# Optimization experiments

Measured on AMD Instinct MI355X. Metric: run time of the kernel, lower is better.

The kernel has to match this reference:

```python
import jax, jax.numpy as jnp
import numpy as np

C_A = 768; C_S = 384; C_Z = 128; H = 16; D = C_A // H
B = 1; N = 4096; NQ = 32; NK = 128; NB = N // NQ
EPS = 1e-5


def _ln(x):
    # layernorm without learned affine (affine applied by caller where present)
    m = jnp.mean(x, axis=-1, keepdims=True)
    v = jnp.mean((x - m) ** 2, axis=-1, keepdims=True)
    return (x - m) * jax.lax.rsqrt(v + EPS)


def setup_inputs() -> dict:
    key = jax.random.key(0)
    ks = jax.random.split(key, 16)
    w = lambda k, shp: jax.random.normal(k, shp, dtype=jnp.float32) * 0.02
    return dict(
        a=jax.random.normal(ks[0], (B, N, C_A), jnp.float32),
        s=jax.random.normal(ks[1], (B, N, C_S), jnp.float32),
        z=jax.random.normal(ks[2], (B, NB, NQ, NK, C_Z), jnp.float32),
        adaln_gamma_s=jnp.ones((C_S,), jnp.float32),
        adaln_ws=w(ks[3], (C_S, C_A)),
        adaln_bs=jnp.zeros((C_A,), jnp.float32),
        adaln_wskip=w(ks[4], (C_S, C_A)),
        lnz_gamma=jnp.ones((C_Z,), jnp.float32),
        wz=w(ks[5], (C_Z, H)),
        wq=w(ks[6], (C_A, C_A)), bq=jnp.zeros((C_A,), jnp.float32),
        wk=w(ks[7], (C_A, C_A)),
        wv=w(ks[8], (C_A, C_A)),
        wg=w(ks[9], (C_A, C_A)), bg=jnp.ones((C_A,), jnp.float32),
        wo=w(ks[10], (C_A, C_A)), bo=jnp.zeros((C_A,), jnp.float32),
        w_last=w(ks[11], (C_S, C_A)),
        b_last=jnp.full((C_A,), -2.0, jnp.float32),  # biasinit = -2.0
        n_queries=NQ, n_keys=NK,
    )


def _forward(a, s, z, adaln_gamma_s, adaln_ws, adaln_bs, adaln_wskip,
             lnz_gamma, wz, wq, bq, wk, wv, wg, bg, wo, bo,
             w_last, b_last, n_queries, n_keys):
    Bq, Nq, _ = a.shape
    nb = Nq // n_queries
    # AdaptiveLayerNorm (AF3 Alg 26): a <- sigmoid(Lin(s_ln)) * LN(a) + LinNoBias(s_ln)
    s_ln = _ln(s) * adaln_gamma_s
    a_ln = jax.nn.sigmoid(s_ln @ adaln_ws + adaln_bs) * _ln(a) + s_ln @ adaln_wskip
    # pair bias: LN(z) (no offset) -> per-head bias, permuted to [B,H,nb,nq,nk]
    bias = (_ln(z) * lnz_gamma) @ wz                    # [B, nb, nq, nk, H]
    bias = jnp.transpose(bias, (0, 4, 1, 2, 3))          # [B, H, nb, nq, nk]
    # projections (q has bias; k/v no bias)
    q = (a_ln @ wq + bq).reshape(Bq, nb, n_queries, H, D)
    k = (a_ln @ wk).reshape(Bq, Nq, H, D)
    v = (a_ln @ wv).reshape(Bq, Nq, H, D)
    # local window: query block w covers [w*nq, (w+1)*nq); keys are nk centered on it
    start = jnp.arange(nb) * n_queries + n_queries // 2 - n_keys // 2
    kidx = start[:, None] + jnp.arange(n_keys)[None, :]  # [nb, nk]
    valid = (kidx >= 0) & (kidx < Nq)
    kidx = jnp.clip(kidx, 0, Nq - 1)
    k_loc = k[:, kidx]                                    # [B, nb, nk, H, D]
    v_loc = v[:, kidx]
    scale = 1.0 / float(np.sqrt(D))
    scores = jnp.einsum('bwqhd,bwkhd->bhwqk', q, k_loc) * scale + bias
    scores = jnp.where(valid[None, None, :, None, :], scores, -1e9)
    p = jax.nn.softmax(scores, axis=-1)
    o = jnp.einsum('bhwqk,bwkhd->bwqhd', p, v_loc).reshape(Bq, Nq, C_A)
    # gating, output projection, final sigmoid gate from raw s
    o = (jax.nn.sigmoid(a_ln @ wg + bg) * o) @ wo + bo
    return jax.nn.sigmoid(s @ w_last + b_last) * o


def reference(a, s, z, adaln_gamma_s, adaln_ws, adaln_bs, adaln_wskip,
              lnz_gamma, wz, wq, bq, wk, wv, wg, bg, wo, bo,
              w_last, b_last, n_queries, n_keys):
    return _forward(a, s, z, adaln_gamma_s, adaln_ws, adaln_bs, adaln_wskip,
                    lnz_gamma, wz, wq, bq, wk, wv, wg, bg, wo, bo,
                    w_last, b_last, n_queries, n_keys)
```

## Files before the change

kernel.cpp:

```cpp
#include <hip/hip_runtime.h>
#include <hip/hip_bf16.h>
#include <math.h>

#define N_TOK 4096
#define CA 768
#define CS 384
#define CZ 128
#define NHEAD 16
#define DH 48
#define NQW 32
#define NKW 128
#define NBLK 128

typedef __attribute__((ext_vector_type(8))) short short8;
typedef __attribute__((ext_vector_type(4))) float float4v;
typedef __attribute__((ext_vector_type(4))) unsigned short ushort4v;

__device__ __forceinline__ float sigmoidf_(float x){ return 1.0f/(1.0f+__expf(-x)); }

__device__ __forceinline__ unsigned short f2bf(float x){
  unsigned u = __float_as_uint(x);
  unsigned r = (u + 0x7FFFu + ((u>>16)&1u)) >> 16;
  return (unsigned short)r;
}
__device__ __forceinline__ float bf2f(unsigned short b){
  return __uint_as_float(((unsigned)b)<<16);
}
__device__ __forceinline__ short8 cvt8(const float* xv){
  union { short8 v; unsigned short u[8]; } H;
  #pragma unroll
  for (int j=0;j<8;j++) H.u[j] = f2bf(xv[j]);
  return H.v;
}
__device__ __forceinline__ short8 cvt8pk(const float* x){
  union { short8 v; unsigned u32[4]; } H;
  #pragma unroll
  for (int i=0;i<4;i++)
    asm("v_cvt_pk_bf16_f32 %0, %1, %2" : "=v"(H.u32[i]) : "v"(x[2*i]), "v"(x[2*i+1]));
  return H.v;
}

__device__ __forceinline__ void gload_lds16(const void* gsrc, void* ldst){
  __builtin_amdgcn_global_load_lds(
    (const __attribute__((address_space(1))) void*)gsrc,
    (__attribute__((address_space(3))) void*)ldst, 16, 0, 0);
}

__device__ __forceinline__ int xcd_swz(int wg, int nwg){
  int cpx = nwg >> 3;
  return (wg & 7)*cpx + (wg >> 3);
}

__global__ __launch_bounds__(256) void prep_zbias_kernel(
  const float* __restrict__ z, const float* __restrict__ lnz_gamma,
  const float* __restrict__ wz, unsigned short* __restrict__ bias3,
  const float* __restrict__ s, const float* __restrict__ adaln_gamma,
  unsigned short* __restrict__ s_ln_h, unsigned short* __restrict__ s_h,
  const float* __restrict__ a, float* __restrict__ a_n,
  const float* __restrict__ ws, const float* __restrict__ wskip,
  const float* __restrict__ wq, const float* __restrict__ wk,
  const float* __restrict__ wv, const float* __restrict__ wg,
  const float* __restrict__ wo, const float* __restrict__ wlast,
  unsigned short* __restrict__ Wt1, unsigned short* __restrict__ Wt2,
  unsigned short* __restrict__ Wt3, unsigned short* __restrict__ Wt4,
  const float* __restrict__ bq, const float* __restrict__ bg,
  float* __restrict__ biasq)
{
  union PZ {
    float tile[64][65];
    float zbuf[4][2][2048];
  };
  __shared__ PZ sm;
  int bid = blockIdx.x;
  int tid = threadIdx.x;

  if (bid < 1024){
    int wave = tid>>6, lane = tid&63;
    int lr = lane&15, quad = lane>>4;

    short8 bwh[4];
    float w1 = 0.f;
    #pragma unroll
    for (int ks=0;ks<4;ks++){
      float wv_[8];
      #pragma unroll
      for (int j=0;j<8;j++){
        int k = ks*32 + quad*8 + j;
        wv_[j] = wz[k*NHEAD + lr]*lnz_gamma[k];
        w1 += wv_[j];
      }
      bwh[ks] = cvt8pk(wv_);
    }
    w1 += __shfl_xor(w1, 16);
    w1 += __shfl_xor(w1, 32);

    size_t group = (size_t)bid*4 + wave;
    const float* zg = z + group*(size_t)(NKW*CZ);
    unsigned short* outg = bias3 + group*2048;

    int rsub = lane>>5;
    int csw  = lane&31;
    auto stage = [&](int buf, int b){
      #pragma unroll
      for (int i=0;i<8;i++){
        int r  = 2*i + rsub;
        int gc = csw ^ (r & 7);
        gload_lds16(zg + (size_t)(b*16 + r)*CZ + gc*4, &sm.zbuf[wave][buf][i*256]);
      }
    };

    stage(0, 0);
    int buf = 0;
    #pragma unroll 1
    for (int b=0; b<8; ++b){
      if (b < 7){
        stage(buf^1, b+1);
        asm volatile("s_waitcnt vmcnt(8)" ::: "memory");
      } else {
        asm volatile("s_waitcnt vmcnt(0)" ::: "memory");
      }
      __builtin_amdgcn_sched_barrier(0);

      const float* rowp = &sm.zbuf[wave][buf][lr*128];
      int sswz = lr & 7;
      float4 p[8];
      #pragma unroll
      for (int ks=0;ks<4;ks++){
        int c0 = ks*8 + quad*2;
        p[ks*2]   = *(const float4*)(rowp + (size_t)((c0  )^sswz)*4);
        p[ks*2+1] = *(const float4*)(rowp + (size_t)((c0+1)^sswz)*4);
      }
      float sum=0.f, sq=0.f;
      #pragma unroll
      for (int t=0;t<8;t++){
        sum += p[t].x + p[t].y + p[t].z + p[t].w;
        sq  += p[t].x*p[t].x + p[t].y*p[t].y + p[t].z*p[t].z + p[t].w*p[t].w;
      }
      sum += __shfl_xor(sum,16); sum += __shfl_xor(sum,32);
      sq  += __shfl_xor(sq,16);  sq  += __shfl_xor(sq,32);
      float mean = sum*(1.f/CZ);
      float var  = sq*(1.f/CZ) - mean*mean;
      float rs = rsqrtf(var + 1e-5f);

      float4v c = (float4v){0.f,0.f,0.f,0.f};
      #pragma unroll
      for (int ks=0;ks<4;ks++){
        float xv[8];
        xv[0]=p[ks*2].x;   xv[1]=p[ks*2].y;   xv[2]=p[ks*2].z;   xv[3]=p[ks*2].w;
        xv[4]=p[ks*2+1].x; xv[5]=p[ks*2+1].y; xv[6]=p[ks*2+1].z; xv[7]=p[ks*2+1].w;
        c = __builtin_amdgcn_mfma_f32_16x16x32_bf16(cvt8pk(xv), bwh[ks], c, 0,0,0);
      }

      ushort4v o4;
      #pragma unroll
      for (int r=0;r<4;r++){
        int rrow = quad*4 + r;
        float m_r  = __shfl(mean, rrow);
        float rs_r = __shfl(rs, rrow);
        o4[r] = f2bf(rs_r*(c[r] - m_r*w1));
      }
      *(ushort4v*)(outg + lr*128 + b*16 + quad*4) = o4;
      buf ^= 1;
    }
    return;
  }
  bid -= 1024;

  if (bid < 1024){
    int wave = tid>>6, lane = tid&63;
    int row = bid*4 + wave;
    const float* x = s + (size_t)row*CS;
    float v[6]; float sum=0.f, sq=0.f;
    #pragma unroll
    for (int i=0;i<6;i++){ v[i]=x[lane+64*i]; sum+=v[i]; sq+=v[i]*v[i]; }
    #pragma unroll
    for (int off=32; off; off>>=1){ sum+=__shfl_xor(sum,off); sq+=__shfl_xor(sq,off); }
    float m = sum*(1.f/CS);
    float var = sq*(1.f/CS)-m*m;
    float rs = rsqrtf(var+1e-5f);
    #pragma unroll
    for (int i=0;i<6;i++){
      int c = lane+64*i;
      s_ln_h[(size_t)row*CS+c] = f2bf((v[i]-m)*rs*adaln_gamma[c]);
      s_h[(size_t)row*CS+c]    = f2bf(v[i]);
    }
    return;
  }
  bid -= 1024;

  if (bid < 1024){
    int wave = tid>>6, lane = tid&63;
    int row = bid*4 + wave;
    const float* x = a + (size_t)row*CA;
    float v[12]; float sum=0.f, sq=0.f;
    #pragma unroll
    for (int i=0;i<12;i++){ v[i]=x[lane+64*i]; sum+=v[i]; sq+=v[i]*v[i]; }
    #pragma unroll
    for (int off=32; off; off>>=1){ sum+=__shfl_xor(sum,off); sq+=__shfl_xor(sq,off); }
    float m = sum*(1.f/CA);
    float var = sq*(1.f/CA)-m*m;
    float rs = rsqrtf(var+1e-5f);
    float* o = a_n + (size_t)row*CA;
    #pragma unroll
    for (int i=0;i<12;i++) o[lane+64*i] = (v[i]-m)*rs;
    return;
  }
  bid -= 1024;

  if (bid < 936){
    const float* src; unsigned short* dst; int K; int local;
    if      (bid < 72)  { src=ws;    dst=Wt1;                   K=CS; local=bid; }
    else if (bid < 144) { src=wskip; dst=Wt1 + (size_t)768*CS;  K=CS; local=bid-72; }
    else if (bid < 288) { src=wq;    dst=Wt2;                   K=CA; local=bid-144; }
    else if (bid < 432) { src=wk;    dst=Wt2 + (size_t)768*CA;  K=CA; local=bid-288; }
    else if (bid < 576) { src=wv;    dst=Wt2 + (size_t)1536*CA; K=CA; local=bid-432; }
    else if (bid < 720) { src=wg;    dst=Wt2 + (size_t)2304*CA; K=CA; local=bid-576; }
    else if (bid < 864) { src=wo;    dst=Wt3;                   K=CA; local=bid-720; }
    else                { src=wlast; dst=Wt4;                   K=CS; local=bid-864; }
    int ktiles = K/64;
    int kb = (local % ktiles)*64, nb = (local / ktiles)*64;
    int c = tid & 63, r0 = tid >> 6;
    #pragma unroll
    for (int i=0;i<16;i++){
      int r = r0 + 4*i;
      sm.tile[r][c] = src[(size_t)(kb+r)*CA + nb + c];
    }
    __syncthreads();
    #pragma unroll
    for (int i=0;i<16;i++){
      int r = r0 + 4*i;
      dst[(size_t)(nb+r)*K + kb + c] = f2bf(sm.tile[c][r]);
    }
    return;
  }
  bid -= 936;

  int i = bid*256 + tid;
  float v = 0.f;
  if (i < 768) v = bq[i];
  else if (i >= 2304) v = bg[i-2304];
  biasq[i] = v;
}

__global__ __launch_bounds__(256) void adaln_gemm(
  const unsigned short* __restrict__ A, const unsigned short* __restrict__ Bt,
  const float* __restrict__ bs, const float* __restrict__ a_n,
  unsigned short* __restrict__ outh)
{
  __shared__ unsigned short Ash[128*32];
  __shared__ unsigned short B1sh[128*32];
  __shared__ unsigned short B2sh[128*32];

  int tid = threadIdx.x;
  int w = tid >> 6, lane = tid & 63;
  int lr = lane & 15, quad = lane >> 4;
  int wg = xcd_swz(blockIdx.y*gridDim.x + blockIdx.x, gridDim.x*gridDim.y);
  int bx = wg % gridDim.x, by = wg / gridDim.x;
  int m0 = by*128, n0 = bx*128;
  int mbase = (w&1)*64, nbase = (w>>1)*64;

  float4v acc1[4][4], acc2[4][4];
  #pragma unroll
  for (int i=0;i<4;i++)
    #pragma unroll
    for (int j=0;j<4;j++){
      acc1[i][j] = (float4v){0.f,0.f,0.f,0.f};
      acc2[i][j] = (float4v){0.f,0.f,0.f,0.f};
    }

  int grow = w*32 + (lane>>2);
  int gcol8 = (lane&3)*8;

  for (int k0=0; k0<CS; k0+=32){
    __syncthreads();
    #pragma unroll
    for (int i=0;i<2;i++){
      int rA = grow + i*16;
      gload_lds16(A  + (size_t)(m0 + rA)*CS + k0 + gcol8, &Ash[(w*32 + i*16)*32]);
      gload_lds16(Bt + (size_t)(n0 + rA)*CS + k0 + gcol8, &B1sh[(w*32 + i*16)*32]);
      gload_lds16(Bt + (size_t)(768 + n0 + rA)*CS + k0 + gcol8, &B2sh[(w*32 + i*16)*32]);
    }
    __syncthreads();

    short8 af[4], b1f[4], b2f[4];
    #pragma unroll
    for (int mi=0;mi<4;mi++)
      af[mi] = *(const short8*)&Ash[(mbase + mi*16 + lr)*32 + quad*8];
    #pragma unroll
    for (int ni=0;ni<4;ni++){
      b1f[ni] = *(const short8*)&B1sh[(nbase + ni*16 + lr)*32 + quad*8];
      b2f[ni] = *(const short8*)&B2sh[(nbase + ni*16 + lr)*32 + quad*8];
    }
    #pragma unroll
    for (int mi=0;mi<4;mi++)
      #pragma unroll
      for (int ni=0;ni<4;ni++){
        acc1[mi][ni] = __builtin_amdgcn_mfma_f32_16x16x32_bf16(af[mi], b1f[ni], acc1[mi][ni], 0,0,0);
        acc2[mi][ni] = __builtin_amdgcn_mfma_f32_16x16x32_bf16(af[mi], b2f[ni], acc2[mi][ni], 0,0,0);
      }
  }

  #pragma unroll
  for (int ni=0;ni<4;ni++){
    int col = n0 + nbase + ni*16 + lr;
    float bsv = bs[col];
    #pragma unroll
    for (int mi=0;mi<4;mi++){
      #pragma unroll
      for (int reg=0;reg<4;reg++){
        int row = m0 + mbase + mi*16 + quad*4 + reg;
        float v = sigmoidf_(acc1[mi][ni][reg] + bsv)*a_n[(size_t)row*CA + col] + acc2[mi][ni][reg];
        outh[(size_t)row*CA + col] = f2bf(v);
      }
    }
  }
}

template<int MODE>
__global__ __launch_bounds__(256) void gemm_bf16(
  const unsigned short* __restrict__ A1, const unsigned short* __restrict__ B1,
  const float* __restrict__ bias1, int K1,
  const unsigned short* __restrict__ A2, const unsigned short* __restrict__ B2,
  const float* __restrict__ bias2, int K2,
  void* __restrict__ outp, int M, int N)
{
  __shared__ unsigned short Ash[128*32];
  __shared__ unsigned short Bsh[128*32];

  int tid = threadIdx.x;
  int w = tid >> 6, lane = tid & 63;
  int lr = lane & 15, quad = lane >> 4;
  int wg = xcd_swz(blockIdx.y*gridDim.x + blockIdx.x, gridDim.x*gridDim.y);
  int bx = wg % gridDim.x, by = wg / gridDim.x;
  int m0 = by*128, n0 = bx*128;
  int mbase = (w&1)*64, nbase = (w>>1)*64;

  float4v acc1[4][4];
  float4v acc2[4][4];
  #pragma unroll
  for (int i=0;i<4;i++)
    #pragma unroll
    for (int j=0;j<4;j++){
      acc1[i][j] = (float4v){0.f,0.f,0.f,0.f};
      if constexpr (MODE == 3) acc2[i][j] = (float4v){0.f,0.f,0.f,0.f};
    }

  int grow = w*32 + (lane>>2);
  int gcol8 = (lane&3)*8;

  for (int k0=0; k0<K1; k0+=32){
    __syncthreads();
    #pragma unroll
    for (int i=0;i<2;i++){
      int rA = grow + i*16;
      gload_lds16(A1 + (size_t)(m0 + rA)*K1 + k0 + gcol8, &Ash[(w*32 + i*16)*32]);
      gload_lds16(B1 + (size_t)(n0 + rA)*K1 + k0 + gcol8, &Bsh[(w*32 + i*16)*32]);
    }
    __syncthreads();

    short8 af[4], bf[4];
    #pragma unroll
    for (int mi=0;mi<4;mi++)
      af[mi] = *(const short8*)&Ash[(mbase + mi*16 + lr)*32 + quad*8];
    #pragma unroll
    for (int ni=0;ni<4;ni++)
      bf[ni] = *(const short8*)&Bsh[(nbase + ni*16 + lr)*32 + quad*8];
    #pragma unroll
    for (int mi=0;mi<4;mi++)
      #pragma unroll
      for (int ni=0;ni<4;ni++)
        acc1[mi][ni] = __builtin_amdgcn_mfma_f32_16x16x32_bf16(af[mi], bf[ni], acc1[mi][ni], 0,0,0);
  }

  if constexpr (MODE == 3){
    for (int k0=0; k0<K2; k0+=32){
      __syncthreads();
      #pragma unroll
      for (int i=0;i<2;i++){
        int rA = grow + i*16;
        gload_lds16(A2 + (size_t)(m0 + rA)*K2 + k0 + gcol8, &Ash[(w*32 + i*16)*32]);
        gload_lds16(B2 + (size_t)(n0 + rA)*K2 + k0 + gcol8, &Bsh[(w*32 + i*16)*32]);
      }
      __syncthreads();

      short8 af[4], bf[4];
      #pragma unroll
      for (int mi=0;mi<4;mi++)
        af[mi] = *(const short8*)&Ash[(mbase + mi*16 + lr)*32 + quad*8];
      #pragma unroll
      for (int ni=0;ni<4;ni++)
        bf[ni] = *(const short8*)&Bsh[(nbase + ni*16 + lr)*32 + quad*8];
      #pragma unroll
      for (int mi=0;mi<4;mi++)
        #pragma unroll
        for (int ni=0;ni<4;ni++)
          acc2[mi][ni] = __builtin_amdgcn_mfma_f32_16x16x32_bf16(af[mi], bf[ni], acc2[mi][ni], 0,0,0);
    }
  }

  #pragma unroll
  for (int ni=0;ni<4;ni++){
    int col = n0 + nbase + ni*16 + lr;
    float bv1 = bias1 ? bias1[col] : 0.f;
    float bv2 = (MODE==3 && bias2) ? bias2[col] : 0.f;
    #pragma unroll
    for (int mi=0;mi<4;mi++){
      #pragma unroll
      for (int reg=0;reg<4;reg++){
        int row = m0 + mbase + mi*16 + quad*4 + reg;
        float x1 = acc1[mi][ni][reg] + bv1;
        if constexpr (MODE == 1)
          ((unsigned short*)outp)[(size_t)row*N + col] = f2bf(x1);
        else
          ((float*)outp)[(size_t)row*N + col] = sigmoidf_(acc2[mi][ni][reg] + bv2)*x1;
      }
    }
  }
}

__global__ __launch_bounds__(256) void attn_kernel(
  const unsigned short* __restrict__ qh,
  const unsigned short* __restrict__ bias3h,
  unsigned short* __restrict__ og)
{
  __shared__ unsigned short Vs[128*192];
  __shared__ unsigned short Pb[4][32*40];
  int tid = threadIdx.x, wave = tid>>6, lane = tid&63;
  int lr = lane&15, quad = lane>>4;
  int w = blockIdx.x, h = blockIdx.y*4 + wave;
  int start = w*NQW - 48;
  const float scale = 0.14433756729740643f;

  {
    int hbase = blockIdx.y*4*DH;
    #pragma unroll
    for (int it=0; it<12; ++it){
      int c = it*256 + tid;
      int key = c/24, cc = c - key*24;
      int kr = min(max(start+key,0),N_TOK-1);
      short8 v = *(const short8*)&qh[(size_t)kr*3072 + 1536 + hbase + cc*8];
      int cs = cc ^ (((key>>3)&3)*2);
      *(short8*)&Vs[key*192 + cs*8] = v;
    }
  }

  short8 zero8 = {0,0,0,0,0,0,0,0};

  short8 aq[2][2];
  #pragma unroll
  for (int mt=0;mt<2;mt++){
    int row = w*NQW + mt*16 + lr;
    const unsigned short* qp = qh + (size_t)row*3072 + h*DH;
    aq[mt][0] = *(const short8*)(qp + quad*8);
    aq[mt][1] = (quad<2) ? *(const short8*)(qp + 32 + quad*8) : zero8;
  }

  float4v c[2][8];
  #pragma unroll
  for (int mt=0;mt<2;mt++)
    #pragma unroll
    for (int nt=0;nt<8;nt++) c[mt][nt] = (float4v){0.f,0.f,0.f,0.f};

  #pragma unroll 2
  for (int nt=0;nt<8;nt++){
    int krc = min(max(start + nt*16 + lr,0),N_TOK-1);
    const unsigned short* kp = qh + (size_t)krc*3072 + 768 + h*DH;
    short8 bk0 = *(const short8*)(kp + quad*8);
    short8 bk1 = (quad<2) ? *(const short8*)(kp + 32 + quad*8) : zero8;
    #pragma unroll
    for (int mt=0;mt<2;mt++){
      c[mt][nt] = __builtin_amdgcn_mfma_f32_16x16x32_bf16(aq[mt][0], bk0, c[mt][nt], 0,0,0);
      c[mt][nt] = __builtin_amdgcn_mfma_f32_16x16x32_bf16(aq[mt][1], bk1, c[mt][nt], 0,0,0);
    }
  }

  float rmax[2][4], rsum[2][4];
  #pragma unroll
  for (int mt=0;mt<2;mt++)
    #pragma unroll
    for (int r=0;r<4;r++){ rmax[mt][r] = -3.0e38f; rsum[mt][r] = 0.f; }

  #pragma unroll
  for (int nt=0;nt<8;nt++){
    int key = start + nt*16 + lr;
    bool valid = (key>=0) && (key<N_TOK);
    #pragma unroll
    for (int mt=0;mt<2;mt++){
      #pragma unroll
      for (int r=0;r<4;r++){
        int q = mt*16 + quad*4 + r;
        float bv = bf2f(bias3h[(((size_t)(w*NQW+q))*NHEAD + h)*128 + nt*16 + lr]);
        float v = valid ? (c[mt][nt][r]*scale + bv) : -1e9f;
        c[mt][nt][r] = v;
        rmax[mt][r] = fmaxf(rmax[mt][r], v);
      }
    }
  }
  #pragma unroll
  for (int mt=0;mt<2;mt++)
    #pragma unroll
    for (int r=0;r<4;r++){
      float m = rmax[mt][r];
      m = fmaxf(m, __shfl_xor(m,1)); m = fmaxf(m, __shfl_xor(m,2));
      m = fmaxf(m, __shfl_xor(m,4)); m = fmaxf(m, __shfl_xor(m,8));
      rmax[mt][r] = m;
    }
  #pragma unroll
  for (int nt=0;nt<8;nt++)
    #pragma unroll
    for (int mt=0;mt<2;mt++)
      #pragma unroll
      for (int r=0;r<4;r++){
        float e = __expf(c[mt][nt][r] - rmax[mt][r]);
        c[mt][nt][r] = e;
        rsum[mt][r] += e;
      }
  #pragma unroll
  for (int mt=0;mt<2;mt++)
    #pragma unroll
    for (int r=0;r<4;r++){
      float sv = rsum[mt][r];
      sv += __shfl_xor(sv,1); sv += __shfl_xor(sv,2);
      sv += __shfl_xor(sv,4); sv += __shfl_xor(sv,8);
      rsum[mt][r] = 1.f/sv;
    }

  __syncthreads();

  unsigned short* ph = &Pb[wave][0];
  float4v o[2][3];
  #pragma unroll
  for (int mt=0;mt<2;mt++)
    #pragma unroll
    for (int no=0;no<3;no++) o[mt][no] = (float4v){0.f,0.f,0.f,0.f};

  #pragma unroll 1
  for (int c2=0;c2<2;c2++){
    #pragma unroll 1
    for (int ks=0;ks<2;ks++){
      int ntb = c2*4 + ks*2;
      #pragma unroll
      for (int t=0;t<2;t++){
        int nt = ntb + t;
        #pragma unroll
        for (int mt=0;mt<2;mt++){
          #pragma unroll
          for (int r=0;r<4;r++){
            int q = mt*16 + quad*4 + r;
            ph[q*40 + t*16 + lr] = f2bf(c[mt][nt][r]*rsum[mt][r]);
          }
        }
      }
      short8 pa[2];
      #pragma unroll
      for (int mt=0;mt<2;mt++)
        pa[mt] = *(const short8*)&ph[(mt*16+lr)*40 + quad*8];
      #pragma unroll
      for (int no=0;no<3;no++){
        union { short8 v; unsigned short u[8]; } V;
        int col = wave*DH + no*16 + lr;
        int chunk = col >> 3;
        int cs = (chunk ^ (quad*2))*8 + (col & 7);
        #pragma unroll
        for (int j=0;j<8;j++){
          int key = c2*64 + ks*32 + quad*8 + j;
          V.u[j] = Vs[key*192 + cs];
        }
        #pragma unroll
        for (int mt=0;mt<2;mt++)
          o[mt][no] = __builtin_amdgcn_mfma_f32_16x16x32_bf16(pa[mt], V.v, o[mt][no], 0,0,0);
      }
    }
  }

  #pragma unroll
  for (int mt=0;mt<2;mt++){
    #pragma unroll
    for (int no=0;no<3;no++){
      int d = no*16 + lr;
      #pragma unroll
      for (int r=0;r<4;r++){
        int q = mt*16 + quad*4 + r;
        size_t grow = (size_t)(w*NQW + q);
        float g = bf2f(qh[grow*3072 + 2304 + h*DH + d]);
        og[grow*CA + h*DH + d] = f2bf(o[mt][no][r] * sigmoidf_(g));
      }
    }
  }
}

extern "C" void kernel_launch(void* const* d_in, const int* in_sizes, int n_in,
                              void* d_out, int out_size, void* d_ws, size_t ws_size,
                              hipStream_t stream)
{
  const float* a            = (const float*)d_in[0];
  const float* s            = (const float*)d_in[1];
  const float* z            = (const float*)d_in[2];
  const float* adaln_gamma  = (const float*)d_in[3];
  const float* adaln_ws     = (const float*)d_in[4];
  const float* adaln_bs     = (const float*)d_in[5];
  const float* adaln_wskip  = (const float*)d_in[6];
  const float* lnz_gamma    = (const float*)d_in[7];
  const float* wz           = (const float*)d_in[8];
  const float* wq           = (const float*)d_in[9];
  const float* bq           = (const float*)d_in[10];
  const float* wk           = (const float*)d_in[11];
  const float* wv           = (const float*)d_in[12];
  const float* wg           = (const float*)d_in[13];
  const float* bg           = (const float*)d_in[14];
  const float* wo           = (const float*)d_in[15];
  const float* bo           = (const float*)d_in[16];
  const float* w_last       = (const float*)d_in[17];
  const float* b_last       = (const float*)d_in[18];
  float* out = (float*)d_out;

  char* base = (char*)d_ws;
  size_t off = 0;
  auto alloc = [&](size_t bytes)->char*{ char* p = base + off; off += (bytes + 255) & ~(size_t)255; return p; };

  unsigned short* s_ln_h = (unsigned short*)alloc((size_t)N_TOK*CS*2);
  unsigned short* s_h    = (unsigned short*)alloc((size_t)N_TOK*CS*2);
  float*          a_n    = (float*)alloc((size_t)N_TOK*CA*4);
  unsigned short* a_ln_h = (unsigned short*)alloc((size_t)N_TOK*CA*2);
  unsigned short* og_h   = (unsigned short*)alloc((size_t)N_TOK*CA*2);
  unsigned short* Wt1    = (unsigned short*)alloc((size_t)1536*CS*2);
  unsigned short* Wt2    = (unsigned short*)alloc((size_t)3072*CA*2);
  unsigned short* Wt3    = (unsigned short*)alloc((size_t)CA*CA*2);
  unsigned short* Wt4    = (unsigned short*)alloc((size_t)CA*CS*2);
  unsigned short* bias3h = (unsigned short*)alloc((size_t)N_TOK*NHEAD*NKW*2);
  unsigned short* qkvg_h = (unsigned short*)alloc((size_t)N_TOK*3072*2);
  float*          biasq  = (float*)alloc((size_t)3072*4);

  prep_zbias_kernel<<<dim3(1024+1024+1024+936+12), 256, 0, stream>>>(
      z, lnz_gamma, wz, bias3h,
      s, adaln_gamma, s_ln_h, s_h, a, a_n,
      adaln_ws, adaln_wskip, wq, wk, wv, wg, wo, w_last,
      Wt1, Wt2, Wt3, Wt4, bq, bg, biasq);

  adaln_gemm<<<dim3(CA/128, N_TOK/128), 256, 0, stream>>>(s_ln_h, Wt1, adaln_bs, a_n, a_ln_h);

  gemm_bf16<1><<<dim3(3072/128, N_TOK/128), 256, 0, stream>>>(
      a_ln_h, Wt2, biasq, CA, nullptr, nullptr, nullptr, 0, qkvg_h, N_TOK, 3072);

  attn_kernel<<<dim3(NBLK, 4), 256, 0, stream>>>(qkvg_h, bias3h, og_h);

  gemm_bf16<3><<<dim3(CA/128, N_TOK/128), 256, 0, stream>>>(
      og_h, Wt3, bo, CA, s_h, Wt4, b_last, CS, out, N_TOK, CA);
}
```

Baseline: 232.8 us.

## Halve GEMM M-tiles for more blocks and split z-bias groups across blocks

The adaln and final GEMMs switch from 128x128 to 64x128 tiles, which doubles the grid from 192 to 384 blocks so more of the GPU's compute units are busy. The final GEMM now merges both K loops into a single loop with a branch. The z-bias prep section now runs with twice as many blocks, and only 2 of the 4 waves in each block do work, which is meant to raise occupancy through the smaller LDS footprint. The QKVG GEMM is specialized with fixed constants. The risks are less data reuse per tile and half-idle blocks in the prep kernel.

Result: faster. 221.0 us (-5.1%).

```diff
diff --git a/kernel.cpp b/kernel.cpp
--- a/kernel.cpp
+++ b/kernel.cpp
@@ -68,14 +68,15 @@
 {
   union PZ {
     float tile[64][65];
-    float zbuf[4][2][2048];
+    float zbuf[2][2][2048];
   };
   __shared__ PZ sm;
   int bid = blockIdx.x;
   int tid = threadIdx.x;
 
-  if (bid < 1024){
+  if (bid < 2048){
     int wave = tid>>6, lane = tid&63;
+    if (wave >= 2) return;
     int lr = lane&15, quad = lane>>4;
 
     short8 bwh[4];
@@ -94,7 +95,7 @@
     w1 += __shfl_xor(w1, 16);
     w1 += __shfl_xor(w1, 32);
 
-    size_t group = (size_t)bid*4 + wave;
+    size_t group = (size_t)bid*2 + wave;
     const float* zg = z + group*(size_t)(NKW*CZ);
     unsigned short* outg = bias3 + group*2048;
 
@@ -164,7 +165,7 @@
     }
     return;
   }
-  bid -= 1024;
+  bid -= 2048;
 
   if (bid < 1024){
     int wave = tid>>6, lane = tid&63;
@@ -247,9 +248,166 @@
   const float* __restrict__ bs, const float* __restrict__ a_n,
   unsigned short* __restrict__ outh)
 {
-  __shared__ unsigned short Ash[128*32];
+  __shared__ unsigned short Ash[64*32];
   __shared__ unsigned short B1sh[128*32];
   __shared__ unsigned short B2sh[128*32];
+
+  int tid = threadIdx.x;
+  int w = tid >> 6, lane = tid & 63;
+  int lr = lane & 15, quad = lane >> 4;
+  int wg = xcd_swz(blockIdx.y*gridDim.x + blockIdx.x, gridDim.x*gridDim.y);
+  int bx = wg % gridDim.x, by = wg / gridDim.x;
+  int m0 = by*64, n0 = bx*128;
+  int mbase = (w&1)*32, nbase = (w>>1)*64;
+
+  float4v acc1[2][4], acc2[2][4];
+  #pragma unroll
+  for (int i=0;i<2;i++)
+    #pragma unroll
+    for (int j=0;j<4;j++){
+      acc1[i][j] = (float4v){0.f,0.f,0.f,0.f};
+      acc2[i][j] = (float4v){0.f,0.f,0.f,0.f};
+    }
+
+  int growB = w*32 + (lane>>2);
+  int growA = w*16 + (lane>>2);
+  int gcol8 = (lane&3)*8;
+
+  for (int k0=0; k0<CS; k0+=32){
+    __syncthreads();
+    gload_lds16(A + (size_t)(m0 + growA)*CS + k0 + gcol8, &Ash[(w*16)*32]);
+    #pragma unroll
+    for (int i=0;i<2;i++){
+      int rB = growB + i*16;
+      gload_lds16(Bt + (size_t)(n0 + rB)*CS + k0 + gcol8, &B1sh[(w*32 + i*16)*32]);
+      gload_lds16(Bt + (size_t)(768 + n0 + rB)*CS + k0 + gcol8, &B2sh[(w*32 + i*16)*32]);
+    }
+    __syncthreads();
+
+    short8 af[2], b1f[4], b2f[4];
+    #pragma unroll
+    for (int mi=0;mi<2;mi++)
+      af[mi] = *(const short8*)&Ash[(mbase + mi*16 + lr)*32 + quad*8];
+    #pragma unroll
+    for (int ni=0;ni<4;ni++){
+      b1f[ni] = *(const short8*)&B1sh[(nbase + ni*16 + lr)*32 + quad*8];
+      b2f[ni] = *(const short8*)&B2sh[(nbase + ni*16 + lr)*32 + quad*8];
+    }
+    #pragma unroll
+    for (int mi=0;mi<2;mi++)
+      #pragma unroll
+      for (int ni=0;ni<4;ni++){
+        acc1[mi][ni] = __builtin_amdgcn_mfma_f32_16x16x32_bf16(af[mi], b1f[ni], acc1[mi][ni], 0,0,0);
+        acc2[mi][ni] = __builtin_amdgcn_mfma_f32_16x16x32_bf16(af[mi], b2f[ni], acc2[mi][ni], 0,0,0);
+      }
+  }
+
+  #pragma unroll
+  for (int ni=0;ni<4;ni++){
+    int col = n0 + nbase + ni*16 + lr;
+    float bsv = bs[col];
+    #pragma unroll
+    for (int mi=0;mi<2;mi++){
+      #pragma unroll
+      for (int reg=0;reg<4;reg++){
+        int row = m0 + mbase + mi*16 + quad*4 + reg;
+        float v = sigmoidf_(acc1[mi][ni][reg] + bsv)*a_n[(size_t)row*CA + col] + acc2[mi][ni][reg];
+        outh[(size_t)row*CA + col] = f2bf(v);
+      }
+    }
+  }
+}
+
+__global__ __launch_bounds__(256) void final_gemm(
+  const unsigned short* __restrict__ A1, const unsigned short* __restrict__ B1,
+  const float* __restrict__ bias1,
+  const unsigned short* __restrict__ A2, const unsigned short* __restrict__ B2,
+  const float* __restrict__ bias2,
+  float* __restrict__ outp)
+{
+  __shared__ unsigned short Ash[64*32];
+  __shared__ unsigned short Bsh[128*32];
+
+  int tid = threadIdx.x;
+  int w = tid >> 6, lane = tid & 63;
+  int lr = lane & 15, quad = lane >> 4;
+  int wg = xcd_swz(blockIdx.y*gridDim.x + blockIdx.x, gridDim.x*gridDim.y);
+  int bx = wg % gridDim.x, by = wg / gridDim.x;
+  int m0 = by*64, n0 = bx*128;
+  int mbase = (w&1)*32, nbase = (w>>1)*64;
+
+  float4v acc1[2][4], acc2[2][4];
+  #pragma unroll
+  for (int i=0;i<2;i++)
+    #pragma unroll
+    for (int j=0;j<4;j++){
+      acc1[i][j] = (float4v){0.f,0.f,0.f,0.f};
+      acc2[i][j] = (float4v){0.f,0.f,0.f,0.f};
+    }
+
+  int growB = w*32 + (lane>>2);
+  int growA = w*16 + (lane>>2);
+  int gcol8 = (lane&3)*8;
+
+  const int NT1 = CA/32, NT2 = CS/32, NT = NT1+NT2;
+  #pragma unroll 1
+  for (int t=0; t<NT; ++t){
+    const unsigned short* Ap; const unsigned short* Bp; int K, k0;
+    if (t < NT1){ Ap=A1; Bp=B1; K=CA; k0=t*32; }
+    else        { Ap=A2; Bp=B2; K=CS; k0=(t-NT1)*32; }
+    __syncthreads();
+    gload_lds16(Ap + (size_t)(m0 + growA)*K + k0 + gcol8, &Ash[(w*16)*32]);
+    #pragma unroll
+    for (int i=0;i<2;i++){
+      int rB = growB + i*16;
+      gload_lds16(Bp + (size_t)(n0 + rB)*K + k0 + gcol8, &Bsh[(w*32 + i*16)*32]);
+    }
+    __syncthreads();
+
+    short8 af[2], bf[4];
+    #pragma unroll
+    for (int mi=0;mi<2;mi++)
+      af[mi] = *(const short8*)&Ash[(mbase + mi*16 + lr)*32 + quad*8];
+    #pragma unroll
+    for (int ni=0;ni<4;ni++)
+      bf[ni] = *(const short8*)&Bsh[(nbase + ni*16 + lr)*32 + quad*8];
+    if (t < NT1){
+      #pragma unroll
+      for (int mi=0;mi<2;mi++)
+        #pragma unroll
+        for (int ni=0;ni<4;ni++)
+          acc1[mi][ni] = __builtin_amdgcn_mfma_f32_16x16x32_bf16(af[mi], bf[ni], acc1[mi][ni], 0,0,0);
+    } else {
+      #pragma unroll
+      for (int mi=0;mi<2;mi++)
+        #pragma unroll
+        for (int ni=0;ni<4;ni++)
+          acc2[mi][ni] = __builtin_amdgcn_mfma_f32_16x16x32_bf16(af[mi], bf[ni], acc2[mi][ni], 0,0,0);
+    }
+  }
+
+  #pragma unroll
+  for (int ni=0;ni<4;ni++){
+    int col = n0 + nbase + ni*16 + lr;
+    float bv1 = bias1[col];
+    float bv2 = bias2[col];
+    #pragma unroll
+    for (int mi=0;mi<2;mi++){
+      #pragma unroll
+      for (int reg=0;reg<4;reg++){
+        int row = m0 + mbase + mi*16 + quad*4 + reg;
+        outp[(size_t)row*CA + col] = sigmoidf_(acc2[mi][ni][reg] + bv2)*(acc1[mi][ni][reg] + bv1);
+      }
+    }
+  }
+}
+
+__global__ __launch_bounds__(256) void qkvg_gemm(
+  const unsigned short* __restrict__ A1, const unsigned short* __restrict__ B1,
+  const float* __restrict__ bias1, unsigned short* __restrict__ outp)
+{
+  __shared__ unsigned short Ash[128*32];
+  __shared__ unsigned short Bsh[128*32];
 
   int tid = threadIdx.x;
   int w = tid >> 6, lane = tid & 63;
@@ -259,160 +417,50 @@
   int m0 = by*128, n0 = bx*128;
   int mbase = (w&1)*64, nbase = (w>>1)*64;
 
-  float4v acc1[4][4], acc2[4][4];
+  float4v acc1[4][4];
   #pragma unroll
   for (int i=0;i<4;i++)
     #pragma unroll
-    for (int j=0;j<4;j++){
+    for (int j=0;j<4;j++)
       acc1[i][j] = (float4v){0.f,0.f,0.f,0.f};
-      acc2[i][j] = (float4v){0.f,0.f,0.f,0.f};
-    }
 
   int grow = w*32 + (lane>>2);
   int gcol8 = (lane&3)*8;
 
-  for (int k0=0; k0<CS; k0+=32){
+  for (int k0=0; k0<CA; k0+=32){
     __syncthreads();
     #pragma unroll
     for (int i=0;i<2;i++){
       int rA = grow + i*16;
-      gload_lds16(A  + (size_t)(m0 + rA)*CS + k0 + gcol8, &Ash[(w*32 + i*16)*32]);
-      gload_lds16(Bt + (size_t)(n0 + rA)*CS + k0 + gcol8, &B1sh[(w*32 + i*16)*32]);
-      gload_lds16(Bt + (size_t)(768 + n0 + rA)*CS + k0 + gcol8, &B2sh[(w*32 + i*16)*32]);
+      gload_lds16(A1 + (size_t)(m0 + rA)*CA + k0 + gcol8, &Ash[(w*32 + i*16)*32]);
+      gload_lds16(B1 + (size_t)(n0 + rA)*CA + k0 + gcol8, &Bsh[(w*32 + i*16)*32]);
     }
     __syncthreads();
 
-    short8 af[4], b1f[4], b2f[4];
+    short8 af[4], bf[4];
     #pragma unroll
     for (int mi=0;mi<4;mi++)
       af[mi] = *(const short8*)&Ash[(mbase + mi*16 + lr)*32 + quad*8];
     #pragma unroll
-    for (int ni=0;ni<4;ni++){
-      b1f[ni] = *(const short8*)&B1sh[(nbase + ni*16 + lr)*32 + quad*8];
-      b2f[ni] = *(const short8*)&B2sh[(nbase + ni*16 + lr)*32 + quad*8];
-    }
+    for (int ni=0;ni<4;ni++)
+      bf[ni] = *(const short8*)&Bsh[(nbase + ni*16 + lr)*32 + quad*8];
     #pragma unroll
     for (int mi=0;mi<4;mi++)
       #pragma unroll
-      for (int ni=0;ni<4;ni++){
-        acc1[mi][ni] = __builtin_amdgcn_mfma_f32_16x16x32_bf16(af[mi], b1f[ni], acc1[mi][ni], 0,0,0);
-        acc2[mi][ni] = __builtin_amdgcn_mfma_f32_16x16x32_bf16(af[mi], b2f[ni], acc2[mi][ni], 0,0,0);
-      }
+      for (int ni=0;ni<4;ni++)
+        acc1[mi][ni] = __builtin_amdgcn_mfma_f32_16x16x32_bf16(af[mi], bf[ni], acc1[mi][ni], 0,0,0);
   }
 
   #pragma unroll
   for (int ni=0;ni<4;ni++){
     int col = n0 + nbase + ni*16 + lr;
-    float bsv = bs[col];
+    float bv = bias1[col];
     #pragma unroll
     for (int mi=0;mi<4;mi++){
       #pragma unroll
       for (int reg=0;reg<4;reg++){
         int row = m0 + mbase + mi*16 + quad*4 + reg;
-        float v = sigmoidf_(acc1[mi][ni][reg] + bsv)*a_n[(size_t)row*CA + col] + acc2[mi][ni][reg];
-        outh[(size_t)row*CA + col] = f2bf(v);
-      }
-    }
-  }
-}
-
-template<int MODE>
-__global__ __launch_bounds__(256) void gemm_bf16(
-  const unsigned short* __restrict__ A1, const unsigned short* __restrict__ B1,
-  const float* __restrict__ bias1, int K1,
-  const unsigned short* __restrict__ A2, const unsigned short* __restrict__ B2,
-  const float* __restrict__ bias2, int K2,
-  void* __restrict__ outp, int M, int N)
-{
-  __shared__ unsigned short Ash[128*32];
-  __shared__ unsigned short Bsh[128*32];
-
-  int tid = threadIdx.x;
-  int w = tid >> 6, lane = tid & 63;
-  int lr = lane & 15, quad = lane >> 4;
-  int wg = xcd_swz(blockIdx.y*gridDim.x + blockIdx.x, gridDim.x*gridDim.y);
-  int bx = wg % gridDim.x, by = wg / gridDim.x;
-  int m0 = by*128, n0 = bx*128;
-  int mbase = (w&1)*64, nbase = (w>>1)*64;
-
-  float4v acc1[4][4];
-  float4v acc2[4][4];
-  #pragma unroll
-  for (int i=0;i<4;i++)
-    #pragma unroll
-    for (int j=0;j<4;j++){
-      acc1[i][j] = (float4v){0.f,0.f,0.f,0.f};
-      if constexpr (MODE == 3) acc2[i][j] = (float4v){0.f,0.f,0.f,0.f};
-    }
-
-  int grow = w*32 + (lane>>2);
-  int gcol8 = (lane&3)*8;
-
-  for (int k0=0; k0<K1; k0+=32){
-    __syncthreads();
-    #pragma unroll
-    for (int i=0;i<2;i++){
-      int rA = grow + i*16;
-      gload_lds16(A1 + (size_t)(m0 + rA)*K1 + k0 + gcol8, &Ash[(w*32 + i*16)*32]);
-      gload_lds16(B1 + (size_t)(n0 + rA)*K1 + k0 + gcol8, &Bsh[(w*32 + i*16)*32]);
-    }
-    __syncthreads();
-
-    short8 af[4], bf[4];
-    #pragma unroll
-    for (int mi=0;mi<4;mi++)
-      af[mi] = *(const short8*)&Ash[(mbase + mi*16 + lr)*32 + quad*8];
-    #pragma unroll
-    for (int ni=0;ni<4;ni++)
-      bf[ni] = *(const short8*)&Bsh[(nbase + ni*16 + lr)*32 + quad*8];
-    #pragma unroll
-    for (int mi=0;mi<4;mi++)
-      #pragma unroll
-      for (int ni=0;ni<4;ni++)
-        acc1[mi][ni] = __builtin_amdgcn_mfma_f32_16x16x32_bf16(af[mi], bf[ni], acc1[mi][ni], 0,0,0);
-  }
-
-  if constexpr (MODE == 3){
-    for (int k0=0; k0<K2; k0+=32){
-      __syncthreads();
-      #pragma unroll
-      for (int i=0;i<2;i++){
-        int rA = grow + i*16;
-        gload_lds16(A2 + (size_t)(m0 + rA)*K2 + k0 + gcol8, &Ash[(w*32 + i*16)*32]);
-        gload_lds16(B2 + (size_t)(n0 + rA)*K2 + k0 + gcol8, &Bsh[(w*32 + i*16)*32]);
-      }
-      __syncthreads();
-
-      short8 af[4], bf[4];
-      #pragma unroll
-      for (int mi=0;mi<4;mi++)
-        af[mi] = *(const short8*)&Ash[(mbase + mi*16 + lr)*32 + quad*8];
-      #pragma unroll
-      for (int ni=0;ni<4;ni++)
-        bf[ni] = *(const short8*)&Bsh[(nbase + ni*16 + lr)*32 + quad*8];
-      #pragma unroll
-      for (int mi=0;mi<4;mi++)
-        #pragma unroll
-        for (int ni=0;ni<4;ni++)
-          acc2[mi][ni] = __builtin_amdgcn_mfma_f32_16x16x32_bf16(af[mi], bf[ni], acc2[mi][ni], 0,0,0);
-    }
-  }
-
-  #pragma unroll
-  for (int ni=0;ni<4;ni++){
-    int col = n0 + nbase + ni*16 + lr;
-    float bv1 = bias1 ? bias1[col] : 0.f;
-    float bv2 = (MODE==3 && bias2) ? bias2[col] : 0.f;
-    #pragma unroll
-    for (int mi=0;mi<4;mi++){
-      #pragma unroll
-      for (int reg=0;reg<4;reg++){
-        int row = m0 + mbase + mi*16 + quad*4 + reg;
-        float x1 = acc1[mi][ni][reg] + bv1;
-        if constexpr (MODE == 1)
-          ((unsigned short*)outp)[(size_t)row*N + col] = f2bf(x1);
-        else
-          ((float*)outp)[(size_t)row*N + col] = sigmoidf_(acc2[mi][ni][reg] + bv2)*x1;
+        outp[(size_t)row*3072 + col] = f2bf(acc1[mi][ni][reg] + bv);
       }
     }
   }
@@ -631,19 +679,18 @@
   unsigned short* qkvg_h = (unsigned short*)alloc((size_t)N_TOK*3072*2);
   float*          biasq  = (float*)alloc((size_t)3072*4);
 
-  prep_zbias_kernel<<<dim3(1024+1024+1024+936+12), 256, 0, stream>>>(
+  prep_zbias_kernel<<<dim3(2048+1024+1024+936+12), 256, 0, stream>>>(
       z, lnz_gamma, wz, bias3h,
       s, adaln_gamma, s_ln_h, s_h, a, a_n,
       adaln_ws, adaln_wskip, wq, wk, wv, wg, wo, w_last,
       Wt1, Wt2, Wt3, Wt4, bq, bg, biasq);
 
-  adaln_gemm<<<dim3(CA/128, N_TOK/128), 256, 0, stream>>>(s_ln_h, Wt1, adaln_bs, a_n, a_ln_h);
-
-  gemm_bf16<1><<<dim3(3072/128, N_TOK/128), 256, 0, stream>>>(
-      a_ln_h, Wt2, biasq, CA, nullptr, nullptr, nullptr, 0, qkvg_h, N_TOK, 3072);
+  adaln_gemm<<<dim3(CA/128, N_TOK/64), 256, 0, stream>>>(s_ln_h, Wt1, adaln_bs, a_n, a_ln_h);
+
+  qkvg_gemm<<<dim3(3072/128, N_TOK/128), 256, 0, stream>>>(a_ln_h, Wt2, biasq, qkvg_h);
 
   attn_kernel<<<dim3(NBLK, 4), 256, 0, stream>>>(qkvg_h, bias3h, og_h);
 
-  gemm_bf16<3><<<dim3(CA/128, N_TOK/128), 256, 0, stream>>>(
-      og_h, Wt3, bo, CA, s_h, Wt4, b_last, CS, out, N_TOK, CA);
-}
+  final_gemm<<<dim3(CA/128, N_TOK/64), 256, 0, stream>>>(
+      og_h, Wt3, bo, s_h, Wt4, b_last, out);
+}
```
